# Kernel tuning notes

Measured on AMD Instinct MI355X. Metric: run time of the kernel, lower is better.

Reference implementation:

```python
import jax, jax.numpy as jnp
import numpy as np

B, S, I, Hd = 128, 512, 128, 512


def setup_inputs() -> dict:
    key = jax.random.key(0)
    ks = jax.random.split(key, 6)
    s_i = 1.0 / np.sqrt(I)
    s_h = 1.0 / np.sqrt(Hd)
    return {
        "x": jax.random.normal(ks[0], (B, S, I), jnp.float32),
        "w_emb": jax.random.uniform(ks[1], (Hd, I), jnp.float32, -s_i, s_i),
        "b_emb": jax.random.uniform(ks[2], (Hd,), jnp.float32, -s_i, s_i),
        "w_ih": jax.random.uniform(ks[3], (3 * Hd, Hd), jnp.float32, -s_h, s_h),
        "b_ih": jax.random.uniform(ks[4], (3 * Hd,), jnp.float32, -s_h, s_h),
        "b_hh": jax.random.uniform(ks[5], (3 * Hd,), jnp.float32, -s_h, s_h),
    }


def reference(x, w_emb, b_emb, w_ih, b_ih, b_hh):
    # Original loop runs one GRU step per timestep with hidden state reset to
    # zero every call, so every step is independent -> fully batched over time.
    # With h=0 the recurrent matmul W_hh @ h vanishes; only b_hh survives.
    emb = jnp.einsum('bsi,hi->bsh', x, w_emb) + b_emb          # [B,S,Hd]
    gi = jnp.einsum('bsh,gh->bsg', emb, w_ih) + b_ih           # [B,S,3Hd]
    ir, iz, inn = jnp.split(gi, 3, axis=-1)
    b_hr, b_hz, b_hn = jnp.split(b_hh, 3)
    r = jax.nn.sigmoid(ir + b_hr)
    z = jax.nn.sigmoid(iz + b_hz)
    n = jnp.tanh(inn + r * b_hn)
    h = (1.0 - z) * n                                          # h' = (1-z)*n + z*0
    H = h[:, :-1, :]               # [B, S-1, Hd]
    h_last = h[:, -1, :][None]     # [1, B, Hd] (num_layers*dirs = 1)
    return (H, h_last)
```

## Files before the change

kernel.cpp:

```cpp
#include <hip/hip_runtime.h>
#include <hip/hip_bf16.h>
#include <stdint.h>

#define M_TOT   65536
#define I_DIM   128
#define HD      512
#define HOFF    33488896
#define HROW    261632

typedef __bf16 bf16x8 __attribute__((ext_vector_type(8)));
typedef float f32x4 __attribute__((ext_vector_type(4)));

struct __align__(8) bf16x4_t { __hip_bfloat16 v[4]; };

__device__ __forceinline__ void async_load16(const void* g, void* l) {
  __builtin_amdgcn_global_load_lds(
      (const __attribute__((address_space(1))) void*)g,
      (__attribute__((address_space(3))) void*)l, 16, 0, 0);
}

__device__ __forceinline__ float fastrcp(float x) {
  return __builtin_amdgcn_rcpf(x);
}
__device__ __forceinline__ float sigf(float x) {
  return fastrcp(1.0f + __expf(-x));
}
__device__ __forceinline__ float tanhfast(float x) {
  return 1.0f - 2.0f * fastrcp(__expf(2.0f * x) + 1.0f);
}

#define PB_X   8192
#define PB_WI  768
#define PB_TR  16
#define PB_BF  384
__global__ void prep(const float* __restrict__ x,
                     const float* __restrict__ we,
                     const float* __restrict__ wi,
                     const float* __restrict__ b_emb,
                     const float* __restrict__ b_ih,
                     __hip_bfloat16* __restrict__ xb,
                     __hip_bfloat16* __restrict__ weT,
                     __hip_bfloat16* __restrict__ wib,
                     float* __restrict__ bfu) {
  const int bid = blockIdx.x;
  const int tid = threadIdx.x;
  if (bid < PB_X) {
    const int i = bid * 256 + tid;
    const float4 v = ((const float4*)x)[i];
    bf16x4_t o;
    o.v[0] = __float2bfloat16(v.x); o.v[1] = __float2bfloat16(v.y);
    o.v[2] = __float2bfloat16(v.z); o.v[3] = __float2bfloat16(v.w);
    ((bf16x4_t*)xb)[i] = o;
  } else if (bid < PB_X + PB_WI) {
    const int i = (bid - PB_X) * 256 + tid;
    const float4 v = ((const float4*)wi)[i];
    bf16x4_t o;
    o.v[0] = __float2bfloat16(v.x); o.v[1] = __float2bfloat16(v.y);
    o.v[2] = __float2bfloat16(v.z); o.v[3] = __float2bfloat16(v.w);
    ((bf16x4_t*)wib)[i] = o;
  } else if (bid < PB_X + PB_WI + PB_TR) {
    const int b = bid - (PB_X + PB_WI);
    const int i  = b * 8 + (tid >> 5);
    const int h0 = (tid & 31) * 16;
    bf16x8 v0, v1;
#pragma unroll
    for (int j = 0; j < 8; ++j) {
      v0[j] = (__bf16)we[(size_t)(h0 + j) * I_DIM + i];
      v1[j] = (__bf16)we[(size_t)(h0 + 8 + j) * I_DIM + i];
    }
    *(bf16x8*)&weT[(size_t)i * HD + h0] = v0;
    *(bf16x8*)&weT[(size_t)i * HD + h0 + 8] = v1;
  } else {
    const int g = (bid - (PB_X + PB_WI + PB_TR)) * 4 + (tid >> 6);
    const int lane = tid & 63;
    const float4* row = (const float4*)(wi + (size_t)g * HD);
    const float4* be  = (const float4*)b_emb;
    float s = 0.0f;
#pragma unroll
    for (int j = 0; j < 2; ++j) {
      const float4 a = row[lane * 2 + j];
      const float4 b = be[lane * 2 + j];
      s += a.x * b.x + a.y * b.y + a.z * b.z + a.w * b.w;
    }
#pragma unroll
    for (int off = 32; off > 0; off >>= 1) s += __shfl_down(s, off);
    if (lane == 0) bfu[g] = s + b_ih[g];
  }
}

__global__ __launch_bounds__(256, 2) void fuse_gemm(
    const __hip_bfloat16* __restrict__ wib,
    const __hip_bfloat16* __restrict__ weT,
    __hip_bfloat16* __restrict__ wf)
{
  __shared__ __align__(16) __hip_bfloat16 smem[32768];

  const int tid  = threadIdx.x;
  const int w    = tid >> 6;
  const int lane = tid & 63;
  const int g0 = blockIdx.x * 128;
  const int wm = (w >> 1) * 64;
  const int wn = (w & 1) * 64;
  const int lrow = lane >> 3;
  const int gc   = ((lane & 7) ^ lrow) * 8;
  const int l15 = lane & 15;
  const int q   = lane >> 4;
  const int sx  = l15 & 7;

  f32x4 acc[4][4];
#pragma unroll
  for (int i = 0; i < 4; ++i)
#pragma unroll
    for (int j = 0; j < 4; ++j) acc[i][j] = (f32x4)0.0f;

#pragma unroll
  for (int c = 0; c < 4; ++c) {
    const int chunk = w * 4 + c;
    const int row = chunk * 8 + lrow;
    async_load16(wib + (size_t)(g0 + row) * HD + gc, (void*)&smem[chunk * 512]);
    async_load16(weT + (size_t)row * HD + gc, (void*)&smem[8192 + chunk * 512]);
  }
  __syncthreads();

#pragma unroll
  for (int t = 0; t < 8; ++t) {
    const __hip_bfloat16* As = smem + (t & 1) * 16384;
    const __hip_bfloat16* Bs = As + 8192;
    if (t < 7) {
      __hip_bfloat16* An = smem + ((t + 1) & 1) * 16384;
      const int k = (t + 1) * 64;
#pragma unroll
      for (int c = 0; c < 4; ++c) {
        const int chunk = w * 4 + c;
        const int row = chunk * 8 + lrow;
        async_load16(wib + (size_t)(g0 + row) * HD + k + gc, (void*)&An[chunk * 512]);
        async_load16(weT + (size_t)row * HD + k + gc, (void*)&An[8192 + chunk * 512]);
      }
    }
    __builtin_amdgcn_sched_barrier(0);
#pragma unroll
    for (int ks = 0; ks < 2; ++ks) {
      const int s = ((ks * 4 + q) ^ sx) * 8;
      bf16x8 af[4], bfr[4];
#pragma unroll
      for (int mi = 0; mi < 4; ++mi)
        af[mi] = *(const bf16x8*)&As[(wm + mi * 16 + l15) * 64 + s];
#pragma unroll
      for (int ni = 0; ni < 4; ++ni)
        bfr[ni] = *(const bf16x8*)&Bs[(wn + ni * 16 + l15) * 64 + s];
      __builtin_amdgcn_s_setprio(1);
#pragma unroll
      for (int ni = 0; ni < 4; ++ni)
#pragma unroll
        for (int mi = 0; mi < 4; ++mi)
          acc[mi][ni] = __builtin_amdgcn_mfma_f32_16x16x32_bf16(
              af[mi], bfr[ni], acc[mi][ni], 0, 0, 0);
      __builtin_amdgcn_s_setprio(0);
    }
    if (t < 7) __syncthreads();
  }

  __hip_bfloat16* ebuf = &smem[w * 4096];
#pragma unroll
  for (int ni = 0; ni < 4; ++ni)
#pragma unroll
    for (int mi = 0; mi < 4; ++mi)
#pragma unroll
      for (int r = 0; r < 4; ++r)
        ebuf[(mi * 16 + q * 4 + r) * 64 + ni * 16 + l15] =
            __float2bfloat16(acc[mi][ni][r]);
#pragma unroll
  for (int i = 0; i < 8; ++i) {
    const int row  = i * 8 + (lane >> 3);
    const int colb = (lane & 7) * 8;
    const bf16x8 v = *(const bf16x8*)&ebuf[row * 64 + colb];
    *(bf16x8*)&wf[(size_t)(g0 + wm + row) * I_DIM + wn + colb] = v;
  }
}

__device__ __forceinline__ void main_stage(const __hip_bfloat16* __restrict__ xb,
                                           const __hip_bfloat16* __restrict__ wf,
                                           int m0, int h0, int k,
                                           __hip_bfloat16* As, __hip_bfloat16* Bs,
                                           int w, int lrow, int gc) {
#pragma unroll
  for (int c = 0; c < 4; ++c) {
    const int chunk = w * 4 + c;
    async_load16(xb + (size_t)(m0 + chunk * 8 + lrow) * I_DIM + k + gc,
                 (void*)&As[chunk * 512]);
  }
#pragma unroll
  for (int g = 0; g < 3; ++g)
#pragma unroll
    for (int c = 0; c < 2; ++c) {
      const int chunk = w * 2 + c;
      async_load16(wf + (size_t)(g * HD + h0 + chunk * 8 + lrow) * I_DIM + k + gc,
                   (void*)&Bs[g * 4096 + chunk * 512]);
    }
}

__global__ __launch_bounds__(256, 2) void gru_main(
    const __hip_bfloat16* __restrict__ xb,
    const __hip_bfloat16* __restrict__ wf,
    const float* __restrict__ bfu,
    const float* __restrict__ b_hh,
    float* __restrict__ out)
{
  __shared__ __align__(16) char smem[81920];

  const int tid  = threadIdx.x;
  const int w    = tid >> 6;
  const int lane = tid & 63;
  const int m0 = blockIdx.x * 128;
  const int h0 = blockIdx.y * 64;
  const int wm = (w >> 1) * 64;
  const int wn = (w & 1) * 32;
  const int lrow = lane >> 3;
  const int gc   = ((lane & 7) ^ lrow) * 8;
  const int l15 = lane & 15;
  const int q   = lane >> 4;
  const int sx  = l15 & 7;

  f32x4 acc[3][4][2];
#pragma unroll
  for (int g = 0; g < 3; ++g)
#pragma unroll
    for (int i = 0; i < 4; ++i)
#pragma unroll
      for (int j = 0; j < 2; ++j) acc[g][i][j] = (f32x4)0.0f;

  main_stage(xb, wf, m0, h0, 0,
             (__hip_bfloat16*)smem, (__hip_bfloat16*)(smem + 16384),
             w, lrow, gc);
  __syncthreads();

#pragma unroll
  for (int t = 0; t < 2; ++t) {
    const __hip_bfloat16* As = (const __hip_bfloat16*)(smem + (t & 1) * 40960);
    const __hip_bfloat16* Bs = (const __hip_bfloat16*)(smem + (t & 1) * 40960 + 16384);
    if (t == 0)
      main_stage(xb, wf, m0, h0, 64,
                 (__hip_bfloat16*)(smem + 40960),
                 (__hip_bfloat16*)(smem + 40960 + 16384), w, lrow, gc);
    __builtin_amdgcn_sched_barrier(0);
    bf16x8 af[2][4];
#pragma unroll
    for (int ks = 0; ks < 2; ++ks) {
      const int s = ((ks * 4 + q) ^ sx) * 8;
#pragma unroll
      for (int mi = 0; mi < 4; ++mi)
        af[ks][mi] = *(const bf16x8*)&As[(wm + mi * 16 + l15) * 64 + s];
    }
#pragma unroll
    for (int g = 0; g < 3; ++g) {
      bf16x8 b[2][2];
#pragma unroll
      for (int ks = 0; ks < 2; ++ks) {
        const int s = ((ks * 4 + q) ^ sx) * 8;
#pragma unroll
        for (int ni = 0; ni < 2; ++ni)
          b[ks][ni] = *(const bf16x8*)&Bs[g * 4096 + (wn + ni * 16 + l15) * 64 + s];
      }
      __builtin_amdgcn_s_setprio(1);
#pragma unroll
      for (int ks = 0; ks < 2; ++ks)
#pragma unroll
        for (int ni = 0; ni < 2; ++ni)
#pragma unroll
          for (int mi = 0; mi < 4; ++mi)
            acc[g][mi][ni] = __builtin_amdgcn_mfma_f32_16x16x32_bf16(
                af[ks][mi], b[ks][ni], acc[g][mi][ni], 0, 0, 0);
      __builtin_amdgcn_s_setprio(0);
    }
    if (t == 0) __syncthreads();
  }

  float* obuf = (float*)(smem + w * 10240);
#pragma unroll
  for (int ni = 0; ni < 2; ++ni) {
    const int col = h0 + wn + ni * 16 + l15;
    const float br = bfu[col] + b_hh[col];
    const float bz = bfu[HD + col] + b_hh[HD + col];
    const float bn = bfu[2 * HD + col];
    const float bhn = b_hh[2 * HD + col];
#pragma unroll
    for (int mi = 0; mi < 4; ++mi) {
#pragma unroll
      for (int r = 0; r < 4; ++r) {
        const float rr = sigf(acc[0][mi][ni][r] + br);
        const float zz = sigf(acc[1][mi][ni][r] + bz);
        const float nn = tanhfast(acc[2][mi][ni][r] + bn + rr * bhn);
        obuf[(mi * 16 + q * 4 + r) * 40 + ni * 16 + l15] = (1.0f - zz) * nn;
      }
    }
  }
  const int srow = lane >> 3;
  const int scol = (lane & 7) * 4;
#pragma unroll
  for (int i = 0; i < 8; ++i) {
    const int row = i * 8 + srow;
    const float4 v = *(const float4*)&obuf[row * 40 + scol];
    const int m = m0 + wm + row;
    const int b = m >> 9;
    const int s = m & 511;
    float* dst = (s < 511)
        ? out + (size_t)b * HROW + (size_t)s * HD + h0 + wn + scol
        : out + (size_t)HOFF + (size_t)b * HD + h0 + wn + scol;
    *(float4*)dst = v;
  }
}

extern "C" void kernel_launch(void* const* d_in, const int* in_sizes, int n_in,
                              void* d_out, int out_size, void* d_ws, size_t ws_size,
                              hipStream_t stream) {
  const float* x_f     = (const float*)d_in[0];
  const float* w_emb_f = (const float*)d_in[1];
  const float* b_emb   = (const float*)d_in[2];
  const float* w_ih_f  = (const float*)d_in[3];
  const float* b_ih    = (const float*)d_in[4];
  const float* b_hh    = (const float*)d_in[5];
  float* out = (float*)d_out;

  char* ws = (char*)d_ws;
  __hip_bfloat16* x_bf   = (__hip_bfloat16*)(ws);
  __hip_bfloat16* wi_bf  = (__hip_bfloat16*)(ws + 16777216);
  __hip_bfloat16* weT_bf = (__hip_bfloat16*)(ws + 18350080);
  __hip_bfloat16* wf_bf  = (__hip_bfloat16*)(ws + 18481152);
  float*          b_fu   = (float*)(ws + 18874368);

  prep<<<PB_X + PB_WI + PB_TR + PB_BF, 256, 0, stream>>>(
      x_f, w_emb_f, w_ih_f, b_emb, b_ih, x_bf, weT_bf, wi_bf, b_fu);

  fuse_gemm<<<12, 256, 0, stream>>>(wi_bf, weT_bf, wf_bf);

  gru_main<<<dim3(M_TOT / 128, HD / 64), 256, 0, stream>>>(
      x_bf, wf_bf, b_fu, b_hh, out);
}
```

Measured before the change: 212.8 us.

## Keep A tile in registers and loop over all hidden chunks per block

Each block now owns 128 rows of M and iterates over all 16 hidden-column chunks of 32. The x tile (full K=128) is loaded once into registers, and the fused weight tiles are double-buffered in LDS. This removes the repeated x reloads across the former 8 grid columns and cuts launch to 512 blocks, at the cost of a serialized per-block loop with a __syncthreads per chunk and less parallelism per launch.

```diff
diff --git a/kernel.cpp b/kernel.cpp
--- a/kernel.cpp
+++ b/kernel.cpp
@@ -178,25 +178,21 @@
   }
 }
 
-__device__ __forceinline__ void main_stage(const __hip_bfloat16* __restrict__ xb,
-                                           const __hip_bfloat16* __restrict__ wf,
-                                           int m0, int h0, int k,
-                                           __hip_bfloat16* As, __hip_bfloat16* Bs,
-                                           int w, int lrow, int gc) {
-#pragma unroll
-  for (int c = 0; c < 4; ++c) {
-    const int chunk = w * 4 + c;
-    async_load16(xb + (size_t)(m0 + chunk * 8 + lrow) * I_DIM + k + gc,
-                 (void*)&As[chunk * 512]);
-  }
-#pragma unroll
-  for (int g = 0; g < 3; ++g)
-#pragma unroll
-    for (int c = 0; c < 2; ++c) {
-      const int chunk = w * 2 + c;
-      async_load16(wf + (size_t)(g * HD + h0 + chunk * 8 + lrow) * I_DIM + k + gc,
-                   (void*)&Bs[g * 4096 + chunk * 512]);
-    }
+__device__ __forceinline__ void stage_B32(const __hip_bfloat16* __restrict__ wf,
+                                          int hc, char* Bbuf,
+                                          int w, int lrow, int gc) {
+  const int h0 = hc * 32;
+#pragma unroll
+  for (int j = 0; j < 6; ++j) {
+    const int idx = w * 6 + j;
+    const int kh = idx / 12;
+    const int cr = idx % 12;
+    const int r  = cr * 8 + lrow;
+    const int g  = r >> 5;
+    const int hh = r & 31;
+    async_load16(wf + (size_t)(g * HD + h0 + hh) * I_DIM + kh * 64 + gc,
+                 (void*)&((__hip_bfloat16*)Bbuf)[kh * 6144 + cr * 512]);
+  }
 }
 
 __global__ __launch_bounds__(256, 2) void gru_main(
@@ -207,106 +203,112 @@
     float* __restrict__ out)
 {
   __shared__ __align__(16) char smem[81920];
+  __hip_bfloat16* A0 = (__hip_bfloat16*)smem;
 
   const int tid  = threadIdx.x;
   const int w    = tid >> 6;
   const int lane = tid & 63;
   const int m0 = blockIdx.x * 128;
-  const int h0 = blockIdx.y * 64;
-  const int wm = (w >> 1) * 64;
-  const int wn = (w & 1) * 32;
+  const int wm = w * 32;
   const int lrow = lane >> 3;
   const int gc   = ((lane & 7) ^ lrow) * 8;
   const int l15 = lane & 15;
   const int q   = lane >> 4;
   const int sx  = l15 & 7;
 
-  f32x4 acc[3][4][2];
-#pragma unroll
-  for (int g = 0; g < 3; ++g)
-#pragma unroll
-    for (int i = 0; i < 4; ++i)
-#pragma unroll
-      for (int j = 0; j < 2; ++j) acc[g][i][j] = (f32x4)0.0f;
-
-  main_stage(xb, wf, m0, h0, 0,
-             (__hip_bfloat16*)smem, (__hip_bfloat16*)(smem + 16384),
-             w, lrow, gc);
+#pragma unroll
+  for (int kh = 0; kh < 2; ++kh)
+#pragma unroll
+    for (int c = 0; c < 4; ++c) {
+      const int chunk = w * 4 + c;
+      async_load16(xb + (size_t)(m0 + chunk * 8 + lrow) * I_DIM + kh * 64 + gc,
+                   (void*)&A0[kh * 8192 + chunk * 512]);
+    }
+  stage_B32(wf, 0, smem + 32768, w, lrow, gc);
   __syncthreads();
 
-#pragma unroll
-  for (int t = 0; t < 2; ++t) {
-    const __hip_bfloat16* As = (const __hip_bfloat16*)(smem + (t & 1) * 40960);
-    const __hip_bfloat16* Bs = (const __hip_bfloat16*)(smem + (t & 1) * 40960 + 16384);
-    if (t == 0)
-      main_stage(xb, wf, m0, h0, 64,
-                 (__hip_bfloat16*)(smem + 40960),
-                 (__hip_bfloat16*)(smem + 40960 + 16384), w, lrow, gc);
-    __builtin_amdgcn_sched_barrier(0);
-    bf16x8 af[2][4];
-#pragma unroll
-    for (int ks = 0; ks < 2; ++ks) {
-      const int s = ((ks * 4 + q) ^ sx) * 8;
-#pragma unroll
-      for (int mi = 0; mi < 4; ++mi)
-        af[ks][mi] = *(const bf16x8*)&As[(wm + mi * 16 + l15) * 64 + s];
-    }
-#pragma unroll
-    for (int g = 0; g < 3; ++g) {
-      bf16x8 b[2][2];
-#pragma unroll
-      for (int ks = 0; ks < 2; ++ks) {
-        const int s = ((ks * 4 + q) ^ sx) * 8;
-#pragma unroll
-        for (int ni = 0; ni < 2; ++ni)
-          b[ks][ni] = *(const bf16x8*)&Bs[g * 4096 + (wn + ni * 16 + l15) * 64 + s];
-      }
-      __builtin_amdgcn_s_setprio(1);
-#pragma unroll
-      for (int ks = 0; ks < 2; ++ks)
-#pragma unroll
-        for (int ni = 0; ni < 2; ++ni)
-#pragma unroll
-          for (int mi = 0; mi < 4; ++mi)
-            acc[g][mi][ni] = __builtin_amdgcn_mfma_f32_16x16x32_bf16(
-                af[ks][mi], b[ks][ni], acc[g][mi][ni], 0, 0, 0);
-      __builtin_amdgcn_s_setprio(0);
-    }
-    if (t == 0) __syncthreads();
-  }
-
-  float* obuf = (float*)(smem + w * 10240);
-#pragma unroll
-  for (int ni = 0; ni < 2; ++ni) {
-    const int col = h0 + wn + ni * 16 + l15;
-    const float br = bfu[col] + b_hh[col];
-    const float bz = bfu[HD + col] + b_hh[HD + col];
-    const float bn = bfu[2 * HD + col];
-    const float bhn = b_hh[2 * HD + col];
-#pragma unroll
-    for (int mi = 0; mi < 4; ++mi) {
-#pragma unroll
-      for (int r = 0; r < 4; ++r) {
-        const float rr = sigf(acc[0][mi][ni][r] + br);
-        const float zz = sigf(acc[1][mi][ni][r] + bz);
-        const float nn = tanhfast(acc[2][mi][ni][r] + bn + rr * bhn);
-        obuf[(mi * 16 + q * 4 + r) * 40 + ni * 16 + l15] = (1.0f - zz) * nn;
-      }
-    }
-  }
+  bf16x8 af[4][2];
+#pragma unroll
+  for (int ks = 0; ks < 4; ++ks) {
+    const int half = ks >> 1;
+    const int s = (((ks & 1) * 4 + q) ^ sx) * 8;
+#pragma unroll
+    for (int mi = 0; mi < 2; ++mi)
+      af[ks][mi] = *(const bf16x8*)&A0[half * 8192 + (wm + mi * 16 + l15) * 64 + s];
+  }
+  __syncthreads();
+
+  float* obuf = (float*)(smem + w * 8192);
   const int srow = lane >> 3;
   const int scol = (lane & 7) * 4;
-#pragma unroll
-  for (int i = 0; i < 8; ++i) {
-    const int row = i * 8 + srow;
-    const float4 v = *(const float4*)&obuf[row * 40 + scol];
-    const int m = m0 + wm + row;
-    const int b = m >> 9;
-    const int s = m & 511;
-    float* dst = (s < 511)
-        ? out + (size_t)b * HROW + (size_t)s * HD + h0 + wn + scol
-        : out + (size_t)HOFF + (size_t)b * HD + h0 + wn + scol;
-    *(float4*)dst = v;
+
+#pragma unroll 2
+  for (int hc = 0; hc < 16; ++hc) {
+    const __hip_bfloat16* Bs =
+        (const __hip_bfloat16*)(smem + 32768 + (hc & 1) * 24576);
+    if (hc < 15)
+      stage_B32(wf, hc + 1, smem + 32768 + ((hc + 1) & 1) * 24576, w, lrow, gc);
+    __builtin_amdgcn_sched_barrier(0);
+
+    f32x4 acc[3][2][2];
+#pragma unroll
+    for (int g = 0; g < 3; ++g)
+#pragma unroll
+      for (int mi = 0; mi < 2; ++mi)
+#pragma unroll
+        for (int ni = 0; ni < 2; ++ni) acc[g][mi][ni] = (f32x4)0.0f;
+
+    __builtin_amdgcn_s_setprio(1);
+#pragma unroll
+    for (int g = 0; g < 3; ++g)
+#pragma unroll
+      for (int ks = 0; ks < 4; ++ks) {
+        const int half = ks >> 1;
+        const int s = (((ks & 1) * 4 + q) ^ sx) * 8;
+#pragma unroll
+        for (int ni = 0; ni < 2; ++ni) {
+          const bf16x8 bv =
+              *(const bf16x8*)&Bs[half * 6144 + (g * 32 + ni * 16 + l15) * 64 + s];
+#pragma unroll
+          for (int mi = 0; mi < 2; ++mi)
+            acc[g][mi][ni] = __builtin_amdgcn_mfma_f32_16x16x32_bf16(
+                af[ks][mi], bv, acc[g][mi][ni], 0, 0, 0);
+        }
+      }
+    __builtin_amdgcn_s_setprio(0);
+
+    const int h0 = hc * 32;
+#pragma unroll
+    for (int ni = 0; ni < 2; ++ni) {
+      const int col = h0 + ni * 16 + l15;
+      const float br = bfu[col] + b_hh[col];
+      const float bz = bfu[HD + col] + b_hh[HD + col];
+      const float bn = bfu[2 * HD + col];
+      const float bhn = b_hh[2 * HD + col];
+#pragma unroll
+      for (int mi = 0; mi < 2; ++mi) {
+#pragma unroll
+        for (int r = 0; r < 4; ++r) {
+          const float rr = sigf(acc[0][mi][ni][r] + br);
+          const float zz = sigf(acc[1][mi][ni][r] + bz);
+          const float nn = tanhfast(acc[2][mi][ni][r] + bn + rr * bhn);
+          obuf[(mi * 16 + q * 4 + r) * 40 + ni * 16 + l15] = (1.0f - zz) * nn;
+        }
+      }
+    }
+#pragma unroll
+    for (int i = 0; i < 4; ++i) {
+      const int row = i * 8 + srow;
+      const float4 v = *(const float4*)&obuf[row * 40 + scol];
+      const int m = m0 + wm + row;
+      const int b = m >> 9;
+      const int s = m & 511;
+      float* dst = (s < 511)
+          ? out + (size_t)b * HROW + (size_t)s * HD + h0 + scol
+          : out + (size_t)HOFF + (size_t)b * HD + h0 + scol;
+      *(float4*)dst = v;
+    }
+    __syncthreads();
   }
 }
 
@@ -333,6 +335,5 @@
 
   fuse_gemm<<<12, 256, 0, stream>>>(wi_bf, weT_bf, wf_bf);
 
-  gru_main<<<dim3(M_TOT / 128, HD / 64), 256, 0, stream>>>(
-      x_bf, wf_bf, b_fu, b_hh, out);
-}
+  gru_main<<<M_TOT / 128, 256, 0, stream>>>(x_bf, wf_bf, b_fu, b_hh, out);
+}
```

Result: no change. 209.4 us (-1.6%).
